# Kernel optimization log

Measured on AMD Instinct MI355X. Metric: run time of the kernel, lower is better.

Reference implementation:

```python
import jax, jax.numpy as jnp
import numpy as np

IN_FEATURES = 4096
OUT_FEATURES = 4096
MAX_RANK = 32
ALPHA = 32
SCALING = ALPHA / MAX_RANK  # 1.0


def setup_inputs() -> dict:
    key = jax.random.key(0)
    k_x, k_u, k_v = jax.random.split(key, 3)
    x = jax.random.normal(k_x, (4, 2048, IN_FEATURES), dtype=jnp.float32)
    U = jax.random.normal(k_u, (OUT_FEATURES, MAX_RANK), dtype=jnp.float32) * 0.01
    S = jnp.ones((MAX_RANK,), dtype=jnp.float32)
    V = jax.random.normal(k_v, (MAX_RANK, IN_FEATURES), dtype=jnp.float32) * 0.01
    return {"x": x, "U": U, "S": S, "V": V}


def reference(x, U, S, V):
    # Original: W = U @ diag(S) @ V ; out = (x @ W.T) * scaling  (dropout=0 -> Identity)
    # Mathematically identical factored form: ((x @ V^T) * S) @ U^T * scaling.
    h = jnp.einsum('bsi,ri->bsr', x, V)        # [B,S,rank]
    h = h * S                                   # scale by singular values
    out = jnp.einsum('bsr,or->bso', h, U)       # [B,S,out]
    return out * SCALING
```

## Files before the change

kernel.cpp:

```cpp
#include <hip/hip_runtime.h>
#include <hip/hip_bf16.h>

typedef __bf16 bf16x8 __attribute__((ext_vector_type(8)));
typedef float  f32x4  __attribute__((ext_vector_type(4)));

#define IN_F   4096
#define OUT_F  4096
#define RANK   32

__device__ __forceinline__ bf16x8 cvt8(float4 a, float4 b) {
    bf16x8 r;
    r[0] = (__bf16)a.x; r[1] = (__bf16)a.y; r[2] = (__bf16)a.z; r[3] = (__bf16)a.w;
    r[4] = (__bf16)b.x; r[5] = (__bf16)b.y; r[6] = (__bf16)b.z; r[7] = (__bf16)b.w;
    return r;
}

__device__ __forceinline__ void gl_lds16(const float* g, void* l) {
    __builtin_amdgcn_global_load_lds(
        (const __attribute__((address_space(1))) char*)g,
        (__attribute__((address_space(3))) char*)l, 16, 0, 0);
}

template <int KS>
__global__ __launch_bounds__(512, 4)
void lora_h(const float* __restrict__ X, const float* __restrict__ S,
            const float* __restrict__ V, float* __restrict__ Hpart)
{
    constexpr int F    = IN_F / KS;
    constexpr int NCHK = F / 64;

    __shared__ float XL[3][64 * 64];
    __shared__ float VL[3][32 * 64];

    const int tid  = threadIdx.x;
    const int wave = tid >> 6;
    const int lane = tid & 63;
    const int r    = lane & 15;
    const int kg   = lane >> 4;

    const int tt = wave & 3;
    const int rh = wave >> 2;

    const int t0    = blockIdx.x * 64;
    const int fbase = blockIdx.y * F;

    const float sr = S[rh * 16 + r];

    const int srow = lane >> 4;
    const int scol = (lane & 15) * 4;

    auto stage = [&](int c, int nb) {
        const int fc = fbase + ((c + blockIdx.x) & (NCHK - 1)) * 64;
        #pragma unroll
        for (int t = 0; t < 3; ++t) {
            const int inst = wave * 3 + t;
            if (inst < 16) {
                const int row = inst * 4 + srow;
                const int col = scol ^ ((row & 7) << 2);
                gl_lds16(X + (size_t)(t0 + row) * IN_F + fc + col,
                         (void*)&XL[nb][inst * 256]);
            } else {
                const int j   = inst - 16;
                const int row = j * 4 + srow;
                const int col = scol ^ ((row & 7) << 2);
                gl_lds16(V + (size_t)row * IN_F + fc + col,
                         (void*)&VL[nb][j * 256]);
            }
        }
    };

    f32x4 acc = {0.f, 0.f, 0.f, 0.f};

    auto compute = [&](int cur) {
        const int sw = (r & 7) << 2;
        const int xrow = (tt * 16 + r) * 64;
        const int vrow = (rh * 16 + r) * 64;
        #pragma unroll
        for (int s = 0; s < 2; ++s) {
            const int base = s * 32 + kg * 8;
            float4 x0 = *(const float4*)&XL[cur][xrow + ((base)     ^ sw)];
            float4 x1 = *(const float4*)&XL[cur][xrow + ((base + 4) ^ sw)];
            float4 v0 = *(const float4*)&VL[cur][vrow + ((base)     ^ sw)];
            float4 v1 = *(const float4*)&VL[cur][vrow + ((base + 4) ^ sw)];
            acc = __builtin_amdgcn_mfma_f32_16x16x32_bf16(
                      cvt8(x0, x1), cvt8(v0, v1), acc, 0, 0, 0);
        }
    };

    stage(0, 0);
    stage(1, 1);

    for (int c = 0; c < NCHK; ++c) {
        if (c + 2 < NCHK) {
            stage(c + 2, (c + 2) % 3);
            asm volatile("s_waitcnt vmcnt(6)" ::: "memory");
        } else if (c + 1 < NCHK) {
            asm volatile("s_waitcnt vmcnt(3)" ::: "memory");
        } else {
            asm volatile("s_waitcnt vmcnt(0)" ::: "memory");
        }
        __builtin_amdgcn_s_barrier();
        __builtin_amdgcn_sched_barrier(0);
        compute(c % 3);
        __builtin_amdgcn_s_barrier();
    }

    float* Hq = Hpart + ((size_t)blockIdx.y * 8192 + t0) * RANK;
    #pragma unroll
    for (int j = 0; j < 4; ++j) {
        const int tok = tt * 16 + kg * 4 + j;
        Hq[(size_t)tok * RANK + rh * 16 + r] = acc[j] * sr;
    }
}

template <int NKS>
__global__ __launch_bounds__(256)
void lora_hred(const float* __restrict__ Hpart, float* __restrict__ H)
{
    const int idx = blockIdx.x * 256 + threadIdx.x;
    const float4* hp = reinterpret_cast<const float4*>(Hpart);
    float4 v = hp[idx];
    #pragma unroll
    for (int k = 1; k < NKS; ++k) {
        float4 p = hp[(size_t)k * 65536 + idx];
        v.x += p.x; v.y += p.y; v.z += p.z; v.w += p.w;
    }
    reinterpret_cast<float4*>(H)[idx] = v;
}

__global__ __launch_bounds__(256, 4)
void lora_out(const float* __restrict__ H, const float* __restrict__ U,
              float* __restrict__ Out)
{
    __shared__ float Hs[32][33];

    const int tid  = threadIdx.x;
    const int wave = tid >> 6;
    const int lane = tid & 63;
    const int r    = lane & 15;
    const int kg   = lane >> 4;

    const int tt = blockIdx.x >> 2;
    const int cq = blockIdx.x & 3;
    const int t0 = tt * 32;

    {
        float4 v = reinterpret_cast<const float4*>(H + (size_t)t0 * RANK)[tid];
        const int tok = tid >> 3;
        const int rr  = (tid & 7) * 4;
        Hs[tok][rr] = v.x; Hs[tok][rr + 1] = v.y;
        Hs[tok][rr + 2] = v.z; Hs[tok][rr + 3] = v.w;
    }
    __syncthreads();

    bf16x8 hb[2];
    #pragma unroll
    for (int a = 0; a < 2; ++a)
        #pragma unroll
        for (int j = 0; j < 8; ++j) hb[a][j] = (__bf16)Hs[a * 16 + r][kg * 8 + j];

    const int wc0 = cq * 1024 + wave * 256;

    #pragma unroll
    for (int g = 0; g < 4; ++g) {
        float4 u0[4], u1[4];
        #pragma unroll
        for (int b = 0; b < 4; ++b) {
            const float4* up = reinterpret_cast<const float4*>(
                U + (size_t)(wc0 + g * 64 + b * 16 + r) * RANK + kg * 8);
            u0[b] = up[0];
            u1[b] = up[1];
        }
        #pragma unroll
        for (int b = 0; b < 4; ++b) {
            bf16x8 ub = cvt8(u0[b], u1[b]);
            #pragma unroll
            for (int a = 0; a < 2; ++a) {
                f32x4 d = {0.f, 0.f, 0.f, 0.f};
                d = __builtin_amdgcn_mfma_f32_16x16x32_bf16(ub, hb[a], d, 0, 0, 0);
                *reinterpret_cast<float4*>(
                    Out + (size_t)(t0 + a * 16 + r) * OUT_F
                        + wc0 + g * 64 + b * 16 + kg * 4)
                    = *reinterpret_cast<float4*>(&d);
            }
        }
    }
}

extern "C" void kernel_launch(void* const* d_in, const int* in_sizes, int n_in,
                              void* d_out, int out_size, void* d_ws, size_t ws_size,
                              hipStream_t stream) {
    const float* X = (const float*)d_in[0];
    const float* U = (const float*)d_in[1];
    const float* S = (const float*)d_in[2];
    const float* V = (const float*)d_in[3];
    float* Out = (float*)d_out;

    float* H     = (float*)d_ws;
    float* Hpart = (float*)d_ws + 262144;

    if (ws_size >= (size_t)5 * 1024 * 1024) {
        lora_h<4><<<dim3(128, 4), 512, 0, stream>>>(X, S, V, Hpart);
        lora_hred<4><<<256, 256, 0, stream>>>(Hpart, H);
        lora_out<<<1024, 256, 0, stream>>>(H, U, Out);
    } else {
        lora_h<1><<<dim3(128, 1), 512, 0, stream>>>(X, S, V, H);
        lora_out<<<1024, 256, 0, stream>>>(H, U, Out);
    }
}
```

Before: 62.34 us.

## Stage X and V as bf16 in LDS via register loads with larger K chunks

The H kernel stops using direct global-to-LDS fp32 loads. It now loads X through registers, converts it to bf16 and double-buffers it in LDS in 256-wide K chunks. The whole V slice for the block is preloaded once into LDS as bf16. This halves LDS footprint per element, removes repeated V reloads and per-MFMA conversions, and cuts barrier count, but it lowers the occupancy hint to 2 and relies on register prefetch instead of async LDS loads. The small-workspace fallback path is replaced by a naive scalar kernel.

```diff
diff --git a/kernel.cpp b/kernel.cpp
--- a/kernel.cpp
+++ b/kernel.cpp
@@ -1,6 +1,7 @@
 #include <hip/hip_runtime.h>
 #include <hip/hip_bf16.h>
 
+typedef __bf16 bf16x4 __attribute__((ext_vector_type(4)));
 typedef __bf16 bf16x8 __attribute__((ext_vector_type(8)));
 typedef float  f32x4  __attribute__((ext_vector_type(4)));
 
@@ -15,22 +16,22 @@
     return r;
 }
 
-__device__ __forceinline__ void gl_lds16(const float* g, void* l) {
-    __builtin_amdgcn_global_load_lds(
-        (const __attribute__((address_space(1))) char*)g,
-        (__attribute__((address_space(3))) char*)l, 16, 0, 0);
+__device__ __forceinline__ bf16x4 cvt4(float4 a) {
+    bf16x4 r;
+    r[0] = (__bf16)a.x; r[1] = (__bf16)a.y; r[2] = (__bf16)a.z; r[3] = (__bf16)a.w;
+    return r;
 }
 
 template <int KS>
-__global__ __launch_bounds__(512, 4)
+__global__ __launch_bounds__(512, 2)
 void lora_h(const float* __restrict__ X, const float* __restrict__ S,
             const float* __restrict__ V, float* __restrict__ Hpart)
 {
     constexpr int F    = IN_F / KS;
-    constexpr int NCHK = F / 64;
-
-    __shared__ float XL[3][64 * 64];
-    __shared__ float VL[3][32 * 64];
+    constexpr int NCHK = F / 256;
+
+    __shared__ __bf16 VL[32][1024];
+    __shared__ __bf16 XL[2][64][256];
 
     const int tid  = threadIdx.x;
     const int wave = tid >> 6;
@@ -46,63 +47,67 @@
 
     const float sr = S[rh * 16 + r];
 
-    const int srow = lane >> 4;
-    const int scol = (lane & 15) * 4;
-
-    auto stage = [&](int c, int nb) {
-        const int fc = fbase + ((c + blockIdx.x) & (NCHK - 1)) * 64;
-        #pragma unroll
-        for (int t = 0; t < 3; ++t) {
-            const int inst = wave * 3 + t;
-            if (inst < 16) {
-                const int row = inst * 4 + srow;
-                const int col = scol ^ ((row & 7) << 2);
-                gl_lds16(X + (size_t)(t0 + row) * IN_F + fc + col,
-                         (void*)&XL[nb][inst * 256]);
-            } else {
-                const int j   = inst - 16;
-                const int row = j * 4 + srow;
-                const int col = scol ^ ((row & 7) << 2);
-                gl_lds16(V + (size_t)row * IN_F + fc + col,
-                         (void*)&VL[nb][j * 256]);
-            }
+    {
+        float4 vr[16];
+        #pragma unroll
+        for (int t = 0; t < 16; ++t) {
+            const int row = wave * 4 + (t >> 2), q = t & 3;
+            vr[t] = *reinterpret_cast<const float4*>(
+                V + (size_t)row * IN_F + fbase + q * 256 + lane * 4);
+        }
+        #pragma unroll
+        for (int t = 0; t < 16; ++t) {
+            const int row = wave * 4 + (t >> 2), q = t & 3;
+            const int e = (q * 256 + lane * 4) ^ ((row & 7) << 3);
+            *reinterpret_cast<bf16x4*>(&VL[row][e]) = cvt4(vr[t]);
+        }
+    }
+
+    float4 xr[8];
+    auto xload = [&](int c) {
+        const int fc = fbase + ((c + blockIdx.x) & (NCHK - 1)) * 256;
+        #pragma unroll
+        for (int t = 0; t < 8; ++t) {
+            const int row = wave * 8 + t;
+            xr[t] = *reinterpret_cast<const float4*>(
+                X + (size_t)(t0 + row) * IN_F + fc + lane * 4);
         }
     };
+    auto xwrite = [&](int cur) {
+        #pragma unroll
+        for (int t = 0; t < 8; ++t) {
+            const int row = wave * 8 + t;
+            const int e = (lane * 4) ^ ((row & 7) << 3);
+            *reinterpret_cast<bf16x4*>(&XL[cur][row][e]) = cvt4(xr[t]);
+        }
+    };
 
     f32x4 acc = {0.f, 0.f, 0.f, 0.f};
 
-    auto compute = [&](int cur) {
-        const int sw = (r & 7) << 2;
-        const int xrow = (tt * 16 + r) * 64;
-        const int vrow = (rh * 16 + r) * 64;
-        #pragma unroll
-        for (int s = 0; s < 2; ++s) {
-            const int base = s * 32 + kg * 8;
-            float4 x0 = *(const float4*)&XL[cur][xrow + ((base)     ^ sw)];
-            float4 x1 = *(const float4*)&XL[cur][xrow + ((base + 4) ^ sw)];
-            float4 v0 = *(const float4*)&VL[cur][vrow + ((base)     ^ sw)];
-            float4 v1 = *(const float4*)&VL[cur][vrow + ((base + 4) ^ sw)];
-            acc = __builtin_amdgcn_mfma_f32_16x16x32_bf16(
-                      cvt8(x0, x1), cvt8(v0, v1), acc, 0, 0, 0);
+    auto compute = [&](int c, int cur) {
+        const int sw    = (r & 7) << 3;
+        const int vbase = ((c + blockIdx.x) & (NCHK - 1)) * 256;
+        #pragma unroll
+        for (int s = 0; s < 8; ++s) {
+            bf16x8 xb = *reinterpret_cast<const bf16x8*>(
+                &XL[cur][tt * 16 + r][(s * 32 + kg * 8) ^ sw]);
+            bf16x8 vb = *reinterpret_cast<const bf16x8*>(
+                &VL[rh * 16 + r][(vbase + s * 32 + kg * 8) ^ sw]);
+            acc = __builtin_amdgcn_mfma_f32_16x16x32_bf16(xb, vb, acc, 0, 0, 0);
         }
     };
 
-    stage(0, 0);
-    stage(1, 1);
+    xload(0);
+    xwrite(0);
+    __syncthreads();
 
     for (int c = 0; c < NCHK; ++c) {
-        if (c + 2 < NCHK) {
-            stage(c + 2, (c + 2) % 3);
-            asm volatile("s_waitcnt vmcnt(6)" ::: "memory");
-        } else if (c + 1 < NCHK) {
-            asm volatile("s_waitcnt vmcnt(3)" ::: "memory");
-        } else {
-            asm volatile("s_waitcnt vmcnt(0)" ::: "memory");
-        }
-        __builtin_amdgcn_s_barrier();
-        __builtin_amdgcn_sched_barrier(0);
-        compute(c % 3);
-        __builtin_amdgcn_s_barrier();
+        if (c + 1 < NCHK) xload(c + 1);
+        compute(c, c & 1);
+        if (c + 1 < NCHK) {
+            xwrite((c + 1) & 1);
+            __syncthreads();
+        }
     }
 
     float* Hq = Hpart + ((size_t)blockIdx.y * 8192 + t0) * RANK;
@@ -111,6 +116,18 @@
         const int tok = tt * 16 + kg * 4 + j;
         Hq[(size_t)tok * RANK + rh * 16 + r] = acc[j] * sr;
     }
+}
+
+__global__ __launch_bounds__(256)
+void lora_h_naive(const float* __restrict__ X, const float* __restrict__ S,
+                  const float* __restrict__ V, float* __restrict__ H)
+{
+    const int idx = blockIdx.x * 256 + threadIdx.x;
+    const int tok = idx >> 5, rk = idx & 31;
+    float acc = 0.f;
+    for (int f = 0; f < IN_F; ++f)
+        acc += X[(size_t)tok * IN_F + f] * V[(size_t)rk * IN_F + f];
+    H[idx] = acc * S[rk];
 }
 
 template <int NKS>
@@ -204,7 +221,7 @@
         lora_hred<4><<<256, 256, 0, stream>>>(Hpart, H);
         lora_out<<<1024, 256, 0, stream>>>(H, U, Out);
     } else {
-        lora_h<1><<<dim3(128, 1), 512, 0, stream>>>(X, S, V, H);
+        lora_h_naive<<<1024, 256, 0, stream>>>(X, S, V, H);
         lora_out<<<1024, 256, 0, stream>>>(H, U, Out);
     }
 }
```

After: 64.47 us. 1.03x slower.
